# Kernel optimization log

Measured on AMD Instinct MI355X. Metric: run time of the kernel, lower is better.

Reference implementation:

```python
import jax, jax.numpy as jnp
import numpy as np

MAX_POS = 224  # rope cache length (== image_size here)


def build_rope_cache_2d(max_pos, dim, base=10000.0):
    # [max_pos, dim//4, 2] (cos, sin) per axis-position
    half = dim // 2
    theta = 1.0 / base ** (jnp.arange(0, half, 2, dtype=jnp.float32) / half)
    freqs = jnp.arange(max_pos, dtype=jnp.float32)[:, None] * theta[None, :]
    return jnp.stack([jnp.cos(freqs), jnp.sin(freqs)], axis=-1)


def apply_rope_2d(x, coords, rope_cache, image_size):
    B, K, D = x.shape
    half, quarter = D // 2, D // 4
    max_pos = rope_cache.shape[0]
    cn = jnp.clip(coords.astype(jnp.float32) / image_size * (max_pos - 1), 0, max_pos - 1)
    y_pos = cn[..., 0].astype(jnp.int32)
    x_pos = cn[..., 1].astype(jnp.int32)
    y_rope = rope_cache[y_pos]  # [B,K,quarter,2] gather
    x_rope = rope_cache[x_pos]

    def rot(part, r):
        c, s = r[..., 0], r[..., 1]
        p0, p1 = part[..., 0], part[..., 1]
        return jnp.stack([p0 * c - p1 * s, p0 * s + p1 * c], axis=-1).reshape(B, K, half)

    x_part = x[..., :half].reshape(B, K, quarter, 2)
    y_part = x[..., half:].reshape(B, K, quarter, 2)
    return jnp.concatenate([rot(x_part, x_rope), rot(y_part, y_rope)], axis=-1)


def setup_inputs() -> dict:
    key = jax.random.key(0)
    ks = jax.random.split(key, 8)
    B, K, D = 4, 2048, 256
    image_size = 224
    x = jax.random.normal(ks[0], (B, K, D), dtype=jnp.float32)
    coords = jax.random.randint(ks[1], (B, K, 2), 0, image_size).astype(jnp.int32)
    is_context = jax.random.randint(ks[2], (B, K), 0, 2) > 0  # ~half context patches
    scale = 1.0 / np.sqrt(D)
    Wq = jax.random.normal(ks[3], (D, D), jnp.float32) * scale
    Wk = jax.random.normal(ks[4], (D, D), jnp.float32) * scale
    Wv = jax.random.normal(ks[5], (D, D), jnp.float32) * scale
    Wo = jax.random.normal(ks[6], (D, D), jnp.float32) * scale
    bq = jnp.zeros((D,), jnp.float32)
    bk = jnp.zeros((D,), jnp.float32)
    bv = jnp.zeros((D,), jnp.float32)
    bo = jnp.zeros((D,), jnp.float32)
    rope_cache = build_rope_cache_2d(MAX_POS, D)
    return dict(x=x, coords=coords, is_context=is_context, image_size=image_size,
                Wq=Wq, bq=bq, Wk=Wk, bk=bk, Wv=Wv, bv=bv, Wo=Wo, bo=bo,
                rope_cache=rope_cache)


def reference(x, coords, is_context, image_size, Wq, bq, Wk, bk, Wv, bv, Wo, bo, rope_cache):
    H = 8
    B, K, D = x.shape
    hd = D // H
    # 2D RoPE gather + rotation on patch tokens
    xr = apply_rope_2d(x, coords, rope_cache, image_size)
    # q/k/v projections -> [B,H,K,hd]
    q = (xr @ Wq + bq).reshape(B, K, H, hd).transpose(0, 2, 1, 3)
    k = (xr @ Wk + bk).reshape(B, K, H, hd).transpose(0, 2, 1, 3)
    v = (xr @ Wv + bv).reshape(B, K, H, hd).transpose(0, 2, 1, 3)
    scores = jnp.einsum('bhqd,bhkd->bhqk', q, k) * (hd ** -0.5)
    # structured mask: context->context dense block, target->all
    ctx_to_ctx = is_context[:, :, None] & is_context[:, None, :]  # [B,K,K]
    tgt_to_all = (~is_context)[:, :, None]                         # [B,K,1]
    mask = ctx_to_ctx | tgt_to_all
    scores = jnp.where(mask[:, None, :, :], scores, -jnp.inf)
    attn = jax.nn.softmax(scores, axis=-1)
    out = jnp.einsum('bhqk,bhkd->bhqd', attn, v)
    out = out.transpose(0, 2, 1, 3).reshape(B, K, D)
    return out @ Wo + bo
```

## Files before the change

### kernel.cpp

```cpp
#include <hip/hip_runtime.h>
#include <hip/hip_bf16.h>
#include <math.h>

#define BB 4
#define KK 2048
#define DD 256
#define HH 8
#define HD 32
#define HALF 128
#define QUARTER 64

typedef __attribute__((ext_vector_type(8))) short bf16x8;
typedef __attribute__((ext_vector_type(4))) float f32x4;

#define SCALE2F (0.17677669529663687f * 1.4426950408889634f)
#define MASKNEG -3.0e38f

__device__ __forceinline__ ushort f2bf(float f) {
    unsigned u = __builtin_bit_cast(unsigned, f);
    u += 0x7fffu + ((u >> 16) & 1u);
    return (ushort)(u >> 16);
}
__device__ __forceinline__ unsigned pkbf(float a, float b) {
    ushort ua = __builtin_bit_cast(ushort, __float2bfloat16(a));
    ushort ub = __builtin_bit_cast(ushort, __float2bfloat16(b));
    return (unsigned)ua | ((unsigned)ub << 16);
}

__global__ __launch_bounds__(256) void rope_kernel(
    const float* __restrict__ x, const int* __restrict__ coords,
    const float* __restrict__ rope_cache, const int* __restrict__ image_size_p,
    const int* __restrict__ is_ctx, int max_pos,
    ushort* __restrict__ xr16, float* __restrict__ mbias)
{
    int idx = blockIdx.x * blockDim.x + threadIdx.x;
    if (idx >= BB * KK * HALF) return;
    int p   = idx % HALF;
    int row = idx / HALF;

    float img = (float)image_size_p[0];
    float mp1 = (float)(max_pos - 1);
    int c0 = coords[row * 2 + 0];
    int c1 = coords[row * 2 + 1];
    float cy = fminf(fmaxf(((float)c0 / img) * mp1, 0.0f), mp1);
    float cx = fminf(fmaxf(((float)c1 / img) * mp1, 0.0f), mp1);
    int y_pos = (int)cy;
    int x_pos = (int)cx;

    int j, pos, base;
    if (p < QUARTER) { j = p;           pos = x_pos; base = 2 * j; }
    else             { j = p - QUARTER; pos = y_pos; base = HALF + 2 * j; }

    const float* rc = rope_cache + ((size_t)pos * QUARTER + j) * 2;
    float c = rc[0], s = rc[1];
    const float* xin = x + (size_t)row * DD + base;
    float p0 = xin[0], p1 = xin[1];
    unsigned u = (unsigned)f2bf(p0 * c - p1 * s) |
                 ((unsigned)f2bf(p0 * s + p1 * c) << 16);
    *(unsigned*)(xr16 + (size_t)row * DD + base) = u;

    if (p == 0) mbias[row] = (is_ctx[row] != 0) ? 0.0f : MASKNEG;
}

__global__ __launch_bounds__(256) void wprep_kernel(
    const float* __restrict__ Wq, const float* __restrict__ Wk,
    const float* __restrict__ Wv, const float* __restrict__ Wo,
    ushort* __restrict__ wt)
{
    int z = blockIdx.z;
    const float* W = (z == 0) ? Wq : (z == 1) ? Wk : (z == 2) ? Wv : Wo;
    float scale = (z == 0) ? SCALE2F : 1.0f;
    ushort* out = wt + (size_t)z * DD * DD;
    int r0 = blockIdx.x * 64, c0 = blockIdx.y * 64;
    int tid = threadIdx.x;
    __shared__ float t[64][65];
    #pragma unroll
    for (int i = 0; i < 4; ++i) {
        int s  = tid + i * 256;
        int row = s >> 4, c4 = (s & 15) * 4;
        float4 v = *(const float4*)(W + (size_t)(r0 + row) * DD + c0 + c4);
        t[row][c4] = v.x; t[row][c4 + 1] = v.y; t[row][c4 + 2] = v.z; t[row][c4 + 3] = v.w;
    }
    __syncthreads();
    int nl = tid >> 2, ks = (tid & 3) * 16;
    ushort buf[16];
    #pragma unroll
    for (int j = 0; j < 16; ++j) buf[j] = f2bf(t[ks + j][nl] * scale);
    *(uint4*)(out + (size_t)(c0 + nl) * DD + r0 + ks)     = *(uint4*)&buf[0];
    *(uint4*)(out + (size_t)(c0 + nl) * DD + r0 + ks + 8) = *(uint4*)&buf[8];
}

__global__ __launch_bounds__(256) void mfma_gemm_kernel(
    const ushort* __restrict__ A, const ushort* __restrict__ wt,
    const float* __restrict__ b0, const float* __restrict__ b1,
    const float* __restrict__ b2,
    void* __restrict__ o0, void* __restrict__ o1, void* __restrict__ o2,
    int qkv)
{
    int zz = qkv ? blockIdx.z : 3;
    const ushort* Wt = wt + (size_t)zz * DD * DD;
    const float* bp = qkv ? ((blockIdx.z == 0) ? b0 : (blockIdx.z == 1) ? b1 : b2) : b0;
    const int mode = qkv ? ((blockIdx.z == 2) ? 1 : 0) : 2;
    const float bsc = (qkv && blockIdx.z == 0) ? SCALE2F : 1.0f;

    int m0 = blockIdx.x * 128, n0 = blockIdx.y * 64;
    int tid = threadIdx.x;
    int w = tid >> 6, l = tid & 63, lg = l >> 4, ll = l & 15;
    int mrow = m0 + w * 32;

    __shared__ ushort sm[128 * 72];

    f32x4 acc[2][4];
    #pragma unroll
    for (int mt = 0; mt < 2; ++mt)
        #pragma unroll
        for (int nt = 0; nt < 4; ++nt) acc[mt][nt] = (f32x4){0.f, 0.f, 0.f, 0.f};

    const ushort* Ab = A + (size_t)mrow * DD;
    #pragma unroll
    for (int kc = 0; kc < 8; ++kc) {
        bf16x8 af0 = *(const bf16x8*)(Ab + (size_t)ll * DD + kc * 32 + lg * 8);
        bf16x8 af1 = *(const bf16x8*)(Ab + (size_t)(16 + ll) * DD + kc * 32 + lg * 8);
        bf16x8 bfr[4];
        #pragma unroll
        for (int nt = 0; nt < 4; ++nt)
            bfr[nt] = *(const bf16x8*)(Wt + (size_t)(n0 + nt * 16 + ll) * DD + kc * 32 + lg * 8);
        #pragma unroll
        for (int nt = 0; nt < 4; ++nt) {
            acc[0][nt] = __builtin_amdgcn_mfma_f32_16x16x32_bf16(af0, bfr[nt], acc[0][nt], 0, 0, 0);
            acc[1][nt] = __builtin_amdgcn_mfma_f32_16x16x32_bf16(af1, bfr[nt], acc[1][nt], 0, 0, 0);
        }
    }

    float bias[4];
    #pragma unroll
    for (int nt = 0; nt < 4; ++nt) bias[nt] = bp[n0 + nt * 16 + ll] * bsc;

    int bI = m0 >> 11, tokb = m0 & 2047;

    if (mode == 0) {
        #pragma unroll
        for (int mt = 0; mt < 2; ++mt)
            #pragma unroll
            for (int nt = 0; nt < 4; ++nt)
                #pragma unroll
                for (int r = 0; r < 4; ++r)
                    sm[(w * 32 + mt * 16 + lg * 4 + r) * 72 + nt * 16 + ll] =
                        f2bf(acc[mt][nt][r] + bias[nt]);
        __syncthreads();
        ushort* op = (ushort*)((blockIdx.z == 0) ? o0 : o1);
        int h0 = n0 >> 5;
        #pragma unroll
        for (int i = 0; i < 4; ++i) {
            int slot  = tid + i * 256;
            int hh    = slot >> 9;
            int slot2 = slot & 511;
            int tok   = slot2 >> 2, d8 = slot2 & 3;
            uint4 val = *(uint4*)&sm[tok * 72 + hh * 32 + d8 * 8];
            *(uint4*)(op + (((size_t)bI * HH + h0 + hh) * KK + tokb + tok) * HD + d8 * 8) = val;
        }
    } else if (mode == 1) {
        #pragma unroll
        for (int mt = 0; mt < 2; ++mt)
            #pragma unroll
            for (int nt = 0; nt < 4; ++nt)
                #pragma unroll
                for (int r = 0; r < 4; ++r)
                    sm[(nt * 16 + ll) * 136 + w * 32 + mt * 16 + lg * 4 + r] =
                        f2bf(acc[mt][nt][r] + bias[nt]);
        __syncthreads();
        ushort* op = (ushort*)o2;
        #pragma unroll
        for (int i = 0; i < 4; ++i) {
            int slot = tid + i * 256;
            int row  = slot >> 4;
            int t8   = slot & 15;
            uint4 val = *(uint4*)&sm[row * 136 + t8 * 8];
            int n = n0 + row, hI = n >> 5, dI = n & 31;
            *(uint4*)(op + (((size_t)bI * HH + hI) * HD + dI) * KK + tokb + t8 * 8) = val;
        }
    } else {
        float* op = (float*)o0;
        #pragma unroll
        for (int mt = 0; mt < 2; ++mt)
            #pragma unroll
            for (int nt = 0; nt < 4; ++nt)
                #pragma unroll
                for (int r = 0; r < 4; ++r)
                    op[(size_t)(mrow + mt * 16 + lg * 4 + r) * DD + n0 + nt * 16 + ll] =
                        acc[mt][nt][r] + bias[nt];
    }
}

__global__ __launch_bounds__(256, 4) void attn_mfma_kernel(
    const ushort* __restrict__ qb, const ushort* __restrict__ kb,
    const ushort* __restrict__ vt, const int* __restrict__ is_ctx,
    const float* __restrict__ mbias, ushort* __restrict__ ao)
{
    const int b  = blockIdx.z;
    const int h  = blockIdx.y;
    const int bh = b * HH + h;
    const int tid = threadIdx.x;
    const int w  = tid >> 6;
    const int l  = tid & 63;
    const int lg = l >> 4;
    const int ll = l & 15;
    const int q0 = blockIdx.x * 64 + w * 16;

    __shared__ ushort Ks[2][64][40];
    __shared__ ushort Vs[2][32][68];
    __shared__ ushort Pl[4][16][64];
    char* Pw = (char*)&Pl[w][0][0];
    const int sw = (ll & 7) << 4;

    bf16x8 qf = *(const bf16x8*)(qb + ((size_t)bh * KK + q0 + ll) * HD + lg * 8);
    const float qcf = (is_ctx[b * KK + q0 + ll] != 0) ? 1.0f : 0.0f;

    float m = -INFINITY;
    f32x4 acc0 = (f32x4){0.f, 0.f, 0.f, 0.f};
    f32x4 acc1 = (f32x4){0.f, 0.f, 0.f, 0.f};
    f32x4 accl = (f32x4){0.f, 0.f, 0.f, 0.f};

    const ushort* kbase = kb + (size_t)bh * KK * HD;
    const ushort* vbase = vt + (size_t)bh * HD * KK;
    const float*  mbb   = mbias + (size_t)b * KK;
    const f32x4 zero = {0.f, 0.f, 0.f, 0.f};
    const short one = (short)0x3F80;
    const bf16x8 ones = {one, one, one, one, one, one, one, one};

    const int krow = tid >> 2, kblk = tid & 3;
    const int vrow = tid >> 3, vkc  = tid & 7;

    uint4 kreg = *(const uint4*)(kbase + (size_t)krow * HD + kblk * 8);
    uint4 vreg = *(const uint4*)(vbase + (size_t)vrow * KK + vkc * 8);

    int p = 0;
    for (int kt0 = 0; kt0 < KK; kt0 += 64) {
        *(uint4*)&Ks[p][krow][kblk * 8] = kreg;
        *(uint4*)&Vs[p][vrow][vkc * 8]  = vreg;
        __syncthreads();
        if (kt0 + 64 < KK) {
            kreg = *(const uint4*)(kbase + (size_t)(kt0 + 64 + krow) * HD + kblk * 8);
            vreg = *(const uint4*)(vbase + (size_t)vrow * KK + kt0 + 64 + vkc * 8);
        }

        f32x4 st[4];
        float4 mb[4];
        #pragma unroll
        for (int kt = 0; kt < 4; ++kt) {
            bf16x8 kf = *(const bf16x8*)&Ks[p][kt * 16 + ll][lg * 8];
            mb[kt] = *(const float4*)(mbb + kt0 + kt * 16 + lg * 4);
            st[kt] = __builtin_amdgcn_mfma_f32_16x16x32_bf16(kf, qf, zero, 0, 0, 0);
        }
        #pragma unroll
        for (int kt = 0; kt < 4; ++kt) {
            st[kt][0] = fmaf(qcf, mb[kt].x, st[kt][0]);
            st[kt][1] = fmaf(qcf, mb[kt].y, st[kt][1]);
            st[kt][2] = fmaf(qcf, mb[kt].z, st[kt][2]);
            st[kt][3] = fmaf(qcf, mb[kt].w, st[kt][3]);
        }
        float g0 = fmaxf(fmaxf(st[0][0], st[0][1]), st[0][2]);
        float g1 = fmaxf(fmaxf(st[0][3], st[1][0]), st[1][1]);
        float g2 = fmaxf(fmaxf(st[1][2], st[1][3]), st[2][0]);
        float g3 = fmaxf(fmaxf(st[2][1], st[2][2]), st[2][3]);
        float g4 = fmaxf(fmaxf(st[3][0], st[3][1]), st[3][2]);
        float tmax = fmaxf(fmaxf(fmaxf(g0, g1), fmaxf(g2, g3)), fmaxf(g4, st[3][3]));
        tmax = fmaxf(tmax, __shfl_xor(tmax, 16));
        tmax = fmaxf(tmax, __shfl_xor(tmax, 32));

        if (__any(tmax > m + 8.0f)) {
            float mnew = fmaxf(fmaxf(m, tmax), -1e37f);
            float corr = __builtin_amdgcn_exp2f(m - mnew);
            m = mnew;
            #pragma unroll
            for (int r = 0; r < 4; ++r) {
                float cr = __shfl(corr, lg * 4 + r);
                acc0[r] *= cr; acc1[r] *= cr; accl[r] *= cr;
            }
        }
        float msafe = fmaxf(m, -1e37f);

        #pragma unroll
        for (int kt = 0; kt < 4; ++kt) {
            float p0 = __builtin_amdgcn_exp2f(st[kt][0] - msafe);
            float p1 = __builtin_amdgcn_exp2f(st[kt][1] - msafe);
            float p2 = __builtin_amdgcn_exp2f(st[kt][2] - msafe);
            float p3 = __builtin_amdgcn_exp2f(st[kt][3] - msafe);
            uint2 uu;
            uu.x = pkbf(p0, p1);
            uu.y = pkbf(p2, p3);
            *(uint2*)(Pw + ll * 128 + ((kt * 32 + lg * 8) ^ sw)) = uu;
        }

        #pragma unroll
        for (int ks = 0; ks < 2; ++ks) {
            bf16x8 pf = *(const bf16x8*)(Pw + ll * 128 + ((ks * 64 + lg * 16) ^ sw));
            #pragma unroll
            for (int dt = 0; dt < 2; ++dt) {
                bf16x8 vf = *(const bf16x8*)&Vs[p][dt * 16 + ll][ks * 32 + lg * 8];
                if (dt == 0) acc0 = __builtin_amdgcn_mfma_f32_16x16x32_bf16(pf, vf, acc0, 0, 0, 0);
                else         acc1 = __builtin_amdgcn_mfma_f32_16x16x32_bf16(pf, vf, acc1, 0, 0, 0);
            }
            accl = __builtin_amdgcn_mfma_f32_16x16x32_bf16(pf, ones, accl, 0, 0, 0);
        }
        p ^= 1;
    }

    #pragma unroll
    for (int r = 0; r < 4; ++r) {
        float inv = 1.0f / accl[r];
        int q = q0 + lg * 4 + r;
        ushort* orow = ao + ((size_t)b * KK + q) * DD + h * HD;
        orow[ll]      = f2bf(acc0[r] * inv);
        orow[16 + ll] = f2bf(acc1[r] * inv);
    }
}

extern "C" void kernel_launch(void* const* d_in, const int* in_sizes, int n_in,
                              void* d_out, int out_size, void* d_ws, size_t ws_size,
                              hipStream_t stream)
{
    const float* x        = (const float*)d_in[0];
    const int*   coords   = (const int*)  d_in[1];
    const int*   is_ctx   = (const int*)  d_in[2];
    const int*   img_sz   = (const int*)  d_in[3];
    const float* Wq       = (const float*)d_in[4];
    const float* bq       = (const float*)d_in[5];
    const float* Wk       = (const float*)d_in[6];
    const float* bk       = (const float*)d_in[7];
    const float* Wv       = (const float*)d_in[8];
    const float* bv       = (const float*)d_in[9];
    const float* Wo       = (const float*)d_in[10];
    const float* bo       = (const float*)d_in[11];
    const float* rope     = (const float*)d_in[12];

    int max_pos = in_sizes[12] / (QUARTER * 2);

    const size_t NTOK = (size_t)BB * KK;
    const size_t NELT = NTOK * DD;

    char* ws = (char*)d_ws;
    ushort* xr16  = (ushort*)(ws);
    ushort* qbf   = (ushort*)(ws + NELT * 2);
    ushort* kbf   = (ushort*)(ws + NELT * 4);
    ushort* vtbf  = (ushort*)(ws + NELT * 6);
    ushort* ao16  = (ushort*)(ws + NELT * 8);
    ushort* wt    = (ushort*)(ws + NELT * 10);
    float*  mbias = (float*) (ws + NELT * 10 + 524288);
    float* outp = (float*)d_out;

    {
        int total = BB * KK * HALF;
        rope_kernel<<<(total + 255) / 256, 256, 0, stream>>>(
            x, coords, rope, img_sz, is_ctx, max_pos, xr16, mbias);
    }
    wprep_kernel<<<dim3(4, 4, 4), 256, 0, stream>>>(Wq, Wk, Wv, Wo, wt);
    mfma_gemm_kernel<<<dim3(NTOK / 128, DD / 64, 3), 256, 0, stream>>>(
        xr16, wt, bq, bk, bv, qbf, kbf, vtbf, 1);
    attn_mfma_kernel<<<dim3(KK / 64, HH, BB), 256, 0, stream>>>(
        qbf, kbf, vtbf, is_ctx, mbias, ao16);
    mfma_gemm_kernel<<<dim3(NTOK / 128, DD / 64, 1), 256, 0, stream>>>(
        ao16, wt, bo, bo, bo, outp, outp, outp, 0);
}
```

Measured before the change: 165.1 us.

## Stage GEMM tiles through double-buffered LDS and shrink M tile to 64

The projection GEMM kernel now loads A and W tiles cooperatively into double-buffered shared memory, prefetching the next k-chunk into registers while MFMAs run. Before, each wave read its fragments straight from global memory. The M tile drops from 128 to 64 rows, doubling the grid, and the launch bounds are raised for occupancy. This aims to cut redundant global loads of W across waves and improve latency hiding, at the cost of one barrier per k-step.

```diff
diff --git a/kernel.cpp b/kernel.cpp
--- a/kernel.cpp
+++ b/kernel.cpp
@@ -90,7 +90,7 @@
     *(uint4*)(out + (size_t)(c0 + nl) * DD + r0 + ks + 8) = *(uint4*)&buf[8];
 }
 
-__global__ __launch_bounds__(256) void mfma_gemm_kernel(
+__global__ __launch_bounds__(256, 6) void mfma_gemm_kernel(
     const ushort* __restrict__ A, const ushort* __restrict__ wt,
     const float* __restrict__ b0, const float* __restrict__ b1,
     const float* __restrict__ b2,
@@ -103,93 +103,100 @@
     const int mode = qkv ? ((blockIdx.z == 2) ? 1 : 0) : 2;
     const float bsc = (qkv && blockIdx.z == 0) ? SCALE2F : 1.0f;
 
-    int m0 = blockIdx.x * 128, n0 = blockIdx.y * 64;
+    int m0 = blockIdx.x * 64, n0 = blockIdx.y * 64;
     int tid = threadIdx.x;
     int w = tid >> 6, l = tid & 63, lg = l >> 4, ll = l & 15;
-    int mrow = m0 + w * 32;
-
-    __shared__ ushort sm[128 * 72];
-
-    f32x4 acc[2][4];
-    #pragma unroll
-    for (int mt = 0; mt < 2; ++mt)
-        #pragma unroll
-        for (int nt = 0; nt < 4; ++nt) acc[mt][nt] = (f32x4){0.f, 0.f, 0.f, 0.f};
-
-    const ushort* Ab = A + (size_t)mrow * DD;
+
+    __shared__ ushort lds[10240];
+    #define AS_(p, r, k) lds[(p) * 2560 + (r) * 40 + (k)]
+    #define WS_(p, r, k) lds[5120 + (p) * 2560 + (r) * 40 + (k)]
+
+    f32x4 acc[4];
+    #pragma unroll
+    for (int nt = 0; nt < 4; ++nt) acc[nt] = (f32x4){0.f, 0.f, 0.f, 0.f};
+
+    const int srow = tid >> 2, sseg = tid & 3;
+
+    const ushort* Ab = A  + (size_t)(m0 + srow) * DD + sseg * 8;
+    const ushort* Wb = Wt + (size_t)(n0 + srow) * DD + sseg * 8;
+
+    uint4 areg = *(const uint4*)Ab;
+    uint4 wreg = *(const uint4*)Wb;
+
+    int p = 0;
     #pragma unroll
     for (int kc = 0; kc < 8; ++kc) {
-        bf16x8 af0 = *(const bf16x8*)(Ab + (size_t)ll * DD + kc * 32 + lg * 8);
-        bf16x8 af1 = *(const bf16x8*)(Ab + (size_t)(16 + ll) * DD + kc * 32 + lg * 8);
-        bf16x8 bfr[4];
+        *(uint4*)&AS_(p, srow, sseg * 8) = areg;
+        *(uint4*)&WS_(p, srow, sseg * 8) = wreg;
+        __syncthreads();
+        if (kc < 7) {
+            areg = *(const uint4*)(Ab + (kc + 1) * 32);
+            wreg = *(const uint4*)(Wb + (kc + 1) * 32);
+        }
+        bf16x8 af = *(const bf16x8*)&AS_(p, w * 16 + ll, lg * 8);
+        #pragma unroll
+        for (int nt = 0; nt < 4; ++nt) {
+            bf16x8 bfr = *(const bf16x8*)&WS_(p, nt * 16 + ll, lg * 8);
+            acc[nt] = __builtin_amdgcn_mfma_f32_16x16x32_bf16(af, bfr, acc[nt], 0, 0, 0);
+        }
+        p ^= 1;
+    }
+
+    float bias[4];
+    #pragma unroll
+    for (int nt = 0; nt < 4; ++nt) bias[nt] = bp[n0 + nt * 16 + ll] * bsc;
+
+    int bI = m0 >> 11, tokb = m0 & 2047;
+
+    if (mode == 0) {
+        __syncthreads();
         #pragma unroll
         for (int nt = 0; nt < 4; ++nt)
-            bfr[nt] = *(const bf16x8*)(Wt + (size_t)(n0 + nt * 16 + ll) * DD + kc * 32 + lg * 8);
-        #pragma unroll
-        for (int nt = 0; nt < 4; ++nt) {
-            acc[0][nt] = __builtin_amdgcn_mfma_f32_16x16x32_bf16(af0, bfr[nt], acc[0][nt], 0, 0, 0);
-            acc[1][nt] = __builtin_amdgcn_mfma_f32_16x16x32_bf16(af1, bfr[nt], acc[1][nt], 0, 0, 0);
-        }
-    }
-
-    float bias[4];
-    #pragma unroll
-    for (int nt = 0; nt < 4; ++nt) bias[nt] = bp[n0 + nt * 16 + ll] * bsc;
-
-    int bI = m0 >> 11, tokb = m0 & 2047;
-
-    if (mode == 0) {
-        #pragma unroll
-        for (int mt = 0; mt < 2; ++mt)
-            #pragma unroll
-            for (int nt = 0; nt < 4; ++nt)
-                #pragma unroll
-                for (int r = 0; r < 4; ++r)
-                    sm[(w * 32 + mt * 16 + lg * 4 + r) * 72 + nt * 16 + ll] =
-                        f2bf(acc[mt][nt][r] + bias[nt]);
+            #pragma unroll
+            for (int r = 0; r < 4; ++r)
+                lds[(w * 16 + lg * 4 + r) * 72 + nt * 16 + ll] =
+                    f2bf(acc[nt][r] + bias[nt]);
         __syncthreads();
         ushort* op = (ushort*)((blockIdx.z == 0) ? o0 : o1);
         int h0 = n0 >> 5;
         #pragma unroll
-        for (int i = 0; i < 4; ++i) {
-            int slot  = tid + i * 256;
-            int hh    = slot >> 9;
-            int slot2 = slot & 511;
-            int tok   = slot2 >> 2, d8 = slot2 & 3;
-            uint4 val = *(uint4*)&sm[tok * 72 + hh * 32 + d8 * 8];
+        for (int i = 0; i < 2; ++i) {
+            int slot = tid + i * 256;
+            int tok  = slot >> 3, seg = slot & 7;
+            int hh   = seg >> 2, d8 = seg & 3;
+            uint4 val = *(uint4*)&lds[tok * 72 + seg * 8];
             *(uint4*)(op + (((size_t)bI * HH + h0 + hh) * KK + tokb + tok) * HD + d8 * 8) = val;
         }
     } else if (mode == 1) {
-        #pragma unroll
-        for (int mt = 0; mt < 2; ++mt)
-            #pragma unroll
-            for (int nt = 0; nt < 4; ++nt)
-                #pragma unroll
-                for (int r = 0; r < 4; ++r)
-                    sm[(nt * 16 + ll) * 136 + w * 32 + mt * 16 + lg * 4 + r] =
-                        f2bf(acc[mt][nt][r] + bias[nt]);
+        __syncthreads();
+        #pragma unroll
+        for (int nt = 0; nt < 4; ++nt)
+            #pragma unroll
+            for (int r = 0; r < 4; ++r)
+                lds[(nt * 16 + ll) * 72 + w * 16 + lg * 4 + r] =
+                    f2bf(acc[nt][r] + bias[nt]);
         __syncthreads();
         ushort* op = (ushort*)o2;
         #pragma unroll
-        for (int i = 0; i < 4; ++i) {
+        for (int i = 0; i < 2; ++i) {
             int slot = tid + i * 256;
-            int row  = slot >> 4;
-            int t8   = slot & 15;
-            uint4 val = *(uint4*)&sm[row * 136 + t8 * 8];
+            int row  = slot >> 3;
+            int t8   = slot & 7;
+            uint4 val = *(uint4*)&lds[row * 72 + t8 * 8];
             int n = n0 + row, hI = n >> 5, dI = n & 31;
             *(uint4*)(op + (((size_t)bI * HH + hI) * HD + dI) * KK + tokb + t8 * 8) = val;
         }
     } else {
         float* op = (float*)o0;
         #pragma unroll
-        for (int mt = 0; mt < 2; ++mt)
-            #pragma unroll
-            for (int nt = 0; nt < 4; ++nt)
-                #pragma unroll
-                for (int r = 0; r < 4; ++r)
-                    op[(size_t)(mrow + mt * 16 + lg * 4 + r) * DD + n0 + nt * 16 + ll] =
-                        acc[mt][nt][r] + bias[nt];
-    }
+        for (int nt = 0; nt < 4; ++nt)
+            #pragma unroll
+            for (int r = 0; r < 4; ++r)
+                op[(size_t)(m0 + w * 16 + lg * 4 + r) * DD + n0 + nt * 16 + ll] =
+                    acc[nt][r] + bias[nt];
+    }
+    #undef AS_
+    #undef WS_
 }
 
 __global__ __launch_bounds__(256, 4) void attn_mfma_kernel(
@@ -355,10 +362,10 @@
             x, coords, rope, img_sz, is_ctx, max_pos, xr16, mbias);
     }
     wprep_kernel<<<dim3(4, 4, 4), 256, 0, stream>>>(Wq, Wk, Wv, Wo, wt);
-    mfma_gemm_kernel<<<dim3(NTOK / 128, DD / 64, 3), 256, 0, stream>>>(
+    mfma_gemm_kernel<<<dim3(NTOK / 64, DD / 64, 3), 256, 0, stream>>>(
         xr16, wt, bq, bk, bv, qbf, kbf, vtbf, 1);
     attn_mfma_kernel<<<dim3(KK / 64, HH, BB), 256, 0, stream>>>(
         qbf, kbf, vtbf, is_ctx, mbias, ao16);
-    mfma_gemm_kernel<<<dim3(NTOK / 128, DD / 64, 1), 256, 0, stream>>>(
+    mfma_gemm_kernel<<<dim3(NTOK / 64, DD / 64, 1), 256, 0, stream>>>(
         ao16, wt, bo, bo, bo, outp, outp, outp, 0);
 }
```

Result: faster. 155.6 us (-5.7%).
